# Optimization experiments

Measured on AMD Instinct MI355X. Metric: run time of the kernel, lower is better.

Reference implementation:

```python
import jax, jax.numpy as jnp
import numpy as np

H, D = 4, 8          # heads, per-head dim (hidden=32)
HID = 32
NA = 300_000         # addr nodes
NT = 300_000         # tx nodes
E_IN, E_OUT, E_SP = 1_000_000, 1_000_000, 500_000
NLAYERS = 4
NREL = 3


def setup_inputs() -> dict:
    key = jax.random.key(0)
    ks = iter(jax.random.split(key, 40))
    s = 0.1
    inp = {}
    inp['x_addr'] = jax.random.normal(next(ks), (NA, 53), jnp.float32)
    inp['x_tx'] = jax.random.normal(next(ks), (NT, 6), jnp.float32)
    inp['ei_input'] = jax.random.randint(next(ks), (2, E_IN), 0, NA, jnp.int32)   # addr -> tx
    inp['ei_output'] = jax.random.randint(next(ks), (2, E_OUT), 0, NT, jnp.int32)  # tx -> addr
    inp['ei_spent'] = jax.random.randint(next(ks), (2, E_SP), 0, NT, jnp.int32)   # tx -> tx
    # node encoders
    inp['enc_w_addr'] = jax.random.normal(next(ks), (53, HID), jnp.float32) * s
    inp['enc_b_addr'] = jnp.zeros((HID,), jnp.float32)
    inp['enc_w_tx'] = jax.random.normal(next(ks), (6, HID), jnp.float32) * s
    inp['enc_b_tx'] = jnp.zeros((HID,), jnp.float32)
    # layer norms (shared across layers as in the source)
    inp['ln_addr_g'] = jnp.ones((HID,), jnp.float32)
    inp['ln_addr_b'] = jnp.zeros((HID,), jnp.float32)
    inp['ln_tx_g'] = jnp.ones((HID,), jnp.float32)
    inp['ln_tx_b'] = jnp.zeros((HID,), jnp.float32)
    # 4 HANConv layers, params stacked on leading layer axis
    inp['proj_w_addr'] = jax.random.normal(next(ks), (NLAYERS, HID, HID), jnp.float32) * s
    inp['proj_b_addr'] = jnp.zeros((NLAYERS, HID), jnp.float32)
    inp['proj_w_tx'] = jax.random.normal(next(ks), (NLAYERS, HID, HID), jnp.float32) * s
    inp['proj_b_tx'] = jnp.zeros((NLAYERS, HID), jnp.float32)
    inp['att_src'] = jax.random.normal(next(ks), (NLAYERS, NREL, H, D), jnp.float32) * s
    inp['att_dst'] = jax.random.normal(next(ks), (NLAYERS, NREL, H, D), jnp.float32) * s
    inp['klin_w'] = jax.random.normal(next(ks), (NLAYERS, HID, HID), jnp.float32) * s
    inp['klin_b'] = jnp.zeros((NLAYERS, HID), jnp.float32)
    inp['q'] = jax.random.normal(next(ks), (NLAYERS, HID), jnp.float32) * s
    # output head
    inp['lin_w'] = jax.random.normal(next(ks), (HID, 2), jnp.float32) * s
    inp['lin_b'] = jnp.zeros((2,), jnp.float32)
    return inp


def _layernorm(x, g, b, eps=1e-5):
    m = x.mean(-1, keepdims=True)
    v = ((x - m) ** 2).mean(-1, keepdims=True)
    return (x - m) / jnp.sqrt(v + eps) * g + b


def _segment_softmax(alpha, idx, n):
    # alpha: [E, H]; numerically stable softmax over ragged segments (dst nodes)
    amax = jax.ops.segment_max(alpha, idx, num_segments=n)
    amax = jnp.where(jnp.isfinite(amax), amax, 0.0)
    ex = jnp.exp(alpha - amax[idx])
    den = jax.ops.segment_sum(ex, idx, num_segments=n)
    return ex / (den[idx] + 1e-16)


def _han_conv(xa, xt, ei_in, ei_out, ei_sp,
              pw_a, pb_a, pw_t, pb_t, a_src, a_dst, kw, kb, q):
    h_a = (xa @ pw_a + pb_a).reshape(-1, H, D)   # [NA,H,D]
    h_t = (xt @ pw_t + pb_t).reshape(-1, H, D)   # [NT,H,D]
    rels = [(h_a, h_t, ei_in, 0, 'tx'),     # ('addr','input','tx')
            (h_t, h_a, ei_out, 1, 'addr'),  # ('tx','output','addr')
            (h_t, h_t, ei_sp, 2, 'tx')]     # ('tx','spent_output','tx')
    outs = {'addr': [], 'tx': []}
    for hs, hd, ei, t, dname in rels:
        asrc = (hs * a_src[t]).sum(-1)   # [Ns,H]
        adst = (hd * a_dst[t]).sum(-1)   # [Nd,H]
        si, di = ei[0], ei[1]
        e = jax.nn.leaky_relu(asrc[si] + adst[di], negative_slope=0.2)  # [E,H]
        w = _segment_softmax(e, di, hd.shape[0])                        # [E,H]
        msg = hs[si] * w[:, :, None]                                    # [E,H,D]
        agg = jax.ops.segment_sum(msg, di, num_segments=hd.shape[0])
        outs[dname].append(jax.nn.relu(agg.reshape(-1, H * D)))
    def group(xs):
        out = jnp.stack(xs)                                   # [R,N,F]
        score = (q * jnp.tanh(out @ kw + kb).mean(1)).sum(-1)  # [R]
        attn = jax.nn.softmax(score)
        return (attn[:, None, None] * out).sum(0)
    return group(outs['addr']), group(outs['tx'])


def reference(x_addr, x_tx, ei_input, ei_output, ei_spent,
              enc_w_addr, enc_b_addr, enc_w_tx, enc_b_tx,
              ln_addr_g, ln_addr_b, ln_tx_g, ln_tx_b,
              proj_w_addr, proj_b_addr, proj_w_tx, proj_b_tx,
              att_src, att_dst, klin_w, klin_b, q,
              lin_w, lin_b):
    xa = jax.nn.relu(x_addr @ enc_w_addr + enc_b_addr)
    xt = jax.nn.relu(x_tx @ enc_w_tx + enc_b_tx)
    for l in range(NLAYERS):
        oa, ot = _han_conv(xa, xt, ei_input, ei_output, ei_spent,
                           proj_w_addr[l], proj_b_addr[l],
                           proj_w_tx[l], proj_b_tx[l],
                           att_src[l], att_dst[l],
                           klin_w[l], klin_b[l], q[l])
        xa = _layernorm(jax.nn.relu(oa) + xa, ln_addr_g, ln_addr_b)
        xt = _layernorm(jax.nn.relu(ot) + xt, ln_tx_g, ln_tx_b)
    return xa @ lin_w + lin_b
```

## Files before the change

kernel.cpp:

```cpp
#include <hip/hip_runtime.h>
#include <hip/hip_fp16.h>

#define NLAYERS 4
#define BSHIFT 10
#define CHUNK 4096

typedef _Float16 f16x8 __attribute__((ext_vector_type(8)));
typedef float f32x4 __attribute__((ext_vector_type(4)));

__global__ void zero_int_kernel(int* __restrict__ p, long n) {
    long i = (long)blockIdx.x * 256 + threadIdx.x;
    long stride = (long)gridDim.x * 256;
    for (; i < n; i += stride) p[i] = 0;
}

__device__ __forceinline__ float fast_tanh(float y) {
    y = fminf(fmaxf(y, -15.f), 15.f);
    float t = __expf(2.f * y);
    return (t - 1.f) / (t + 1.f);
}

__device__ __forceinline__ int edge_row(const int* ei_in, const int* ei_out, const int* ei_sp,
                                        int E_IN, int E_OUT, int E_SP, int NT, int NA,
                                        int e, int* src) {
    if (e < E_IN) { *src = ei_in[e]; return ei_in[E_IN + e]; }
    if (e < E_IN + E_OUT) { int i = e - E_IN; *src = ei_out[i]; return NT + ei_out[E_OUT + i]; }
    int i = e - E_IN - E_OUT; *src = ei_sp[i]; return NT + NA + ei_sp[E_SP + i];
}

__global__ void hist_kernel(const int* __restrict__ ei_in, const int* __restrict__ ei_out,
                            const int* __restrict__ ei_sp, int E_IN, int E_OUT, int E_SP,
                            int NT, int NA, int* __restrict__ deg, int E_TOT) {
    int e = blockIdx.x * 256 + threadIdx.x;
    if (e >= E_TOT) return;
    int s;
    int row = edge_row(ei_in, ei_out, ei_sp, E_IN, E_OUT, E_SP, NT, NA, e, &s);
    atomicAdd(&deg[row], 1);
}

__global__ void scatter_kernel(const int* __restrict__ ei_in, const int* __restrict__ ei_out,
                               const int* __restrict__ ei_sp, int E_IN, int E_OUT, int E_SP,
                               int NT, int NA, int* __restrict__ cursor, int* __restrict__ col,
                               int E_TOT) {
    int e = blockIdx.x * 256 + threadIdx.x;
    if (e >= E_TOT) return;
    int s;
    int row = edge_row(ei_in, ei_out, ei_sp, E_IN, E_OUT, E_SP, NT, NA, e, &s);
    int pos = atomicAdd(&cursor[row], 1);
    col[pos] = s;
}

__global__ void scan1_kernel(const int* __restrict__ deg, int* __restrict__ rowptr,
                             int* __restrict__ bsum, int n) {
    __shared__ int lds[256];
    int tid = threadIdx.x;
    int base = blockIdx.x * 1024;
    int v[4];
    int mysum = 0;
    #pragma unroll
    for (int j = 0; j < 4; j++) {
        int idx = base + tid * 4 + j;
        v[j] = (idx < n) ? deg[idx] : 0;
        mysum += v[j];
    }
    lds[tid] = mysum;
    __syncthreads();
    for (int off = 1; off < 256; off <<= 1) {
        int t = (tid >= off) ? lds[tid - off] : 0;
        __syncthreads();
        lds[tid] += t;
        __syncthreads();
    }
    int excl = lds[tid] - mysum;
    if (tid == 255) bsum[blockIdx.x] = lds[tid];
    int run = excl;
    #pragma unroll
    for (int j = 0; j < 4; j++) {
        int idx = base + tid * 4 + j;
        if (idx < n) rowptr[idx] = run;
        run += v[j];
    }
}

__global__ void scan2_kernel(int* __restrict__ bsum, int nb) {
    __shared__ int lds[1024];
    int tid = threadIdx.x;
    int v = (tid < nb) ? bsum[tid] : 0;
    lds[tid] = v;
    __syncthreads();
    for (int off = 1; off < 1024; off <<= 1) {
        int t = (tid >= off) ? lds[tid - off] : 0;
        __syncthreads();
        lds[tid] += t;
        __syncthreads();
    }
    if (tid < nb) bsum[tid] = lds[tid] - v;
}

__global__ void scan3_kernel(int* __restrict__ rowptr, const int* __restrict__ bsum,
                             int* __restrict__ cursor, int n, int E) {
    int i = blockIdx.x * 256 + threadIdx.x;
    if (i < n) {
        int r = rowptr[i] + bsum[i >> 10];
        rowptr[i] = r;
        cursor[i] = r;
    }
    if (i == 0) rowptr[n] = E;
}

__global__ void __launch_bounds__(256) bucket_scatter_kernel(
    const int* __restrict__ ei_in, const int* __restrict__ ei_out,
    const int* __restrict__ ei_sp, int E_IN, int E_OUT, int E_SP,
    int NT, int NA, int* __restrict__ bcur,
    uint2* __restrict__ ebuf, int E_TOT, int nbuck, int cap) {
    __shared__ int lc[1024], lbase[1024], lcur[1024];
    int tid = threadIdx.x;
    int chunk0 = blockIdx.x * CHUNK;
    int chunkN = E_TOT - chunk0;
    if (chunkN > CHUNK) chunkN = CHUNK;
    if (chunkN <= 0) return;
    for (int i = tid; i < nbuck; i += 256) { lc[i] = 0; lcur[i] = 0; }
    __syncthreads();
    uint2 er[CHUNK / 256];
    #pragma unroll
    for (int j = 0; j < CHUNK / 256; j++) {
        int i = tid + j * 256;
        if (i < chunkN) {
            int s;
            int row = edge_row(ei_in, ei_out, ei_sp, E_IN, E_OUT, E_SP, NT, NA, chunk0 + i, &s);
            er[j] = make_uint2((unsigned)row, (unsigned)s);
            atomicAdd(&lc[row >> BSHIFT], 1);
        } else {
            er[j].x = 0xFFFFFFFFu;
        }
    }
    __syncthreads();
    for (int i = tid; i < nbuck; i += 256) if (lc[i]) lbase[i] = atomicAdd(&bcur[i], lc[i]);
    __syncthreads();
    #pragma unroll
    for (int j = 0; j < CHUNK / 256; j++) {
        if (er[j].x != 0xFFFFFFFFu) {
            int b = (int)(er[j].x >> BSHIFT);
            int pos = lbase[b] + atomicAdd(&lcur[b], 1);
            if (pos < cap) ebuf[(size_t)b * cap + pos] = er[j];
        }
    }
}

__global__ void scanb_kernel(const int* __restrict__ bcur, int* __restrict__ boff,
                             int* __restrict__ rowptr, int nbuck, int cap, int NCAT) {
    __shared__ int lds[1024];
    int tid = threadIdx.x;
    int v = 0;
    if (tid < nbuck) { v = bcur[tid]; if (v > cap) v = cap; }
    lds[tid] = v;
    __syncthreads();
    for (int off = 1; off < 1024; off <<= 1) {
        int t = (tid >= off) ? lds[tid - off] : 0;
        __syncthreads();
        lds[tid] += t;
        __syncthreads();
    }
    if (tid < nbuck) boff[tid] = lds[tid] - v;
    if (tid == 1023) {
        boff[nbuck] = lds[1023];
        rowptr[NCAT] = lds[1023];
    }
}

__global__ void __launch_bounds__(256) bucket_csr_kernel(
    const uint2* __restrict__ ebuf, const int* __restrict__ boff,
    int* __restrict__ rowptr, int* __restrict__ col, int NCAT, int cap) {
    __shared__ int ldeg[1024];
    __shared__ int lsum[256];
    int tid = threadIdx.x;
    int b = blockIdx.x;
    int row0 = b << BSHIFT;
    int e0 = boff[b], e1 = boff[b + 1];
    int cnt = e1 - e0;
    const uint2* src = ebuf + (size_t)b * cap;
    for (int i = tid; i < 1024; i += 256) ldeg[i] = 0;
    __syncthreads();
    for (int i = tid; i < cnt; i += 256)
        atomicAdd(&ldeg[src[i].x - (unsigned)row0], 1);
    __syncthreads();
    int bidx = tid * 4;
    int v0 = ldeg[bidx], v1 = ldeg[bidx + 1], v2 = ldeg[bidx + 2], v3 = ldeg[bidx + 3];
    int mysum = v0 + v1 + v2 + v3;
    lsum[tid] = mysum;
    __syncthreads();
    for (int off = 1; off < 256; off <<= 1) {
        int t = (tid >= off) ? lsum[tid - off] : 0;
        __syncthreads();
        lsum[tid] += t;
        __syncthreads();
    }
    int run = e0 + lsum[tid] - mysum;
    int vv[4] = {v0, v1, v2, v3};
    #pragma unroll
    for (int j = 0; j < 4; j++) {
        int r = bidx + j;
        if (row0 + r < NCAT) rowptr[row0 + r] = run;
        ldeg[r] = run;
        run += vv[j];
    }
    __syncthreads();
    for (int i = tid; i < cnt; i += 256) {
        uint2 p = src[i];
        int pos = atomicAdd(&ldeg[p.x - (unsigned)row0], 1);
        col[pos] = (int)p.y;
    }
}

__global__ void __launch_bounds__(256) encproj_addr_kernel(
    const float* __restrict__ x,
    const float* __restrict__ We, const float* __restrict__ be,
    const float* __restrict__ Wp, const float* __restrict__ bp,
    const float* __restrict__ a0, const float* __restrict__ a1,
    float* __restrict__ xa, __half* __restrict__ h,
    __half* __restrict__ o0, float* __restrict__ o1,
    int n, int gpb) {
    __shared__ __align__(16) float lds_t[4][16][36];
    __shared__ float sx[4][16 * 57];
    int tid = threadIdx.x;
    int wave = tid >> 6, lane = tid & 63;
    int colid = lane & 15, kgrp = lane >> 4;
    int fbase = kgrp * 8;

    f16x8 bE00, bE01, bE10, bE11;
    #pragma unroll
    for (int j = 0; j < 8; j++) {
        int k0 = fbase + j;
        int k1 = 32 + fbase + j;
        bE00[j] = (_Float16)We[k0 * 32 + colid];
        bE01[j] = (_Float16)We[k0 * 32 + 16 + colid];
        float w10 = (k1 < 53) ? We[k1 * 32 + colid] : 0.f;
        float w11 = (k1 < 53) ? We[k1 * 32 + 16 + colid] : 0.f;
        bE10[j] = (_Float16)w10;
        bE11[j] = (_Float16)w11;
    }
    float beC0 = be[colid], beC1 = be[16 + colid];

    f16x8 bP0, bP1;
    #pragma unroll
    for (int j = 0; j < 8; j++) {
        bP0[j] = (_Float16)Wp[(fbase + j) * 32 + colid];
        bP1[j] = (_Float16)Wp[(fbase + j) * 32 + 16 + colid];
    }
    float bpC0 = bp[colid], bpC1 = bp[16 + colid];

    float va0[8], va1[8];
    #pragma unroll
    for (int j = 0; j < 8; j++) { va0[j] = a0[fbase + j]; va1[j] = a1[fbase + j]; }

    float (*tp)[36] = lds_t[wave];
    float* sxw = sx[wave];
    int blockBase = blockIdx.x * gpb * 64;
    for (int gi = 0; gi < gpb; gi++) {
        int node0 = blockBase + gi * 64 + wave * 16;
        int node = node0 + colid;
        bool valid = node < n;
        int nn = n - node0;
        if (nn > 16) nn = 16;
        if (nn < 0) nn = 0;
        int elems = nn * 53;
        for (int i = lane; i < elems; i += 64) {
            int r = i / 53, c = i - r * 53;
            sxw[r * 57 + c] = x[(size_t)node0 * 53 + i];
        }
        f16x8 af0, af1;
        #pragma unroll
        for (int j = 0; j < 8; j++) {
            af0[j] = (_Float16)sxw[colid * 57 + fbase + j];
            int kk = 32 + fbase + j;
            float v1 = (kk < 53) ? sxw[colid * 57 + kk] : 0.f;
            af1[j] = (_Float16)v1;
        }
        f32x4 c0 = {0.f, 0.f, 0.f, 0.f};
        f32x4 c1 = {0.f, 0.f, 0.f, 0.f};
        c0 = __builtin_amdgcn_mfma_f32_16x16x32_f16(af0, bE00, c0, 0, 0, 0);
        c0 = __builtin_amdgcn_mfma_f32_16x16x32_f16(af1, bE10, c0, 0, 0, 0);
        c1 = __builtin_amdgcn_mfma_f32_16x16x32_f16(af0, bE01, c1, 0, 0, 0);
        c1 = __builtin_amdgcn_mfma_f32_16x16x32_f16(af1, bE11, c1, 0, 0, 0);
        #pragma unroll
        for (int r = 0; r < 4; r++) {
            c0[r] = fmaxf(c0[r] + beC0, 0.f);
            c1[r] = fmaxf(c1[r] + beC1, 0.f);
        }
        #pragma unroll
        for (int r = 0; r < 4; r++) {
            int row = kgrp * 4 + r;
            tp[row][colid] = c0[r];
            tp[row][16 + colid] = c1[r];
        }
        float4 xlo = *(const float4*)&tp[colid][fbase];
        float4 xhi = *(const float4*)&tp[colid][fbase + 4];
        float xe[8] = {xlo.x, xlo.y, xlo.z, xlo.w, xhi.x, xhi.y, xhi.z, xhi.w};
        if (valid) {
            size_t basep = (size_t)node * 32 + fbase;
            *(float4*)(xa + basep) = xlo;
            *(float4*)(xa + basep + 4) = xhi;
        }
        f16x8 af;
        #pragma unroll
        for (int j = 0; j < 8; j++) af[j] = (_Float16)xe[j];
        f32x4 p0 = {0.f, 0.f, 0.f, 0.f};
        f32x4 p1 = {0.f, 0.f, 0.f, 0.f};
        p0 = __builtin_amdgcn_mfma_f32_16x16x32_f16(af, bP0, p0, 0, 0, 0);
        p1 = __builtin_amdgcn_mfma_f32_16x16x32_f16(af, bP1, p1, 0, 0, 0);
        #pragma unroll
        for (int r = 0; r < 4; r++) { p0[r] += bpC0; p1[r] += bpC1; }
        #pragma unroll
        for (int r = 0; r < 4; r++) {
            int row = kgrp * 4 + r;
            tp[row][colid] = p0[r];
            tp[row][16 + colid] = p1[r];
        }
        float4 hlo = *(const float4*)&tp[colid][fbase];
        float4 hhi = *(const float4*)&tp[colid][fbase + 4];
        float hv[8] = {hlo.x, hlo.y, hlo.z, hlo.w, hhi.x, hhi.y, hhi.z, hhi.w};
        if (valid) {
            float4 hout;
            __half2* hp2 = (__half2*)&hout;
            hp2[0] = __floats2half2_rn(hv[0], hv[1]);
            hp2[1] = __floats2half2_rn(hv[2], hv[3]);
            hp2[2] = __floats2half2_rn(hv[4], hv[5]);
            hp2[3] = __floats2half2_rn(hv[6], hv[7]);
            *(float4*)(h + (size_t)node * 32 + fbase) = hout;
            float d0 = 0.f, d1 = 0.f;
            #pragma unroll
            for (int j = 0; j < 8; j++) {
                d0 += hv[j] * va0[j];
                d1 += hv[j] * va1[j];
            }
            size_t oidx = (size_t)node * 4 + kgrp;
            o0[oidx] = __float2half(d0);
            o1[oidx] = d1;
        }
    }
}

__global__ void __launch_bounds__(256) encproj_tx_kernel(
    const float* __restrict__ x,
    const float* __restrict__ We, const float* __restrict__ be,
    const float* __restrict__ Wp, const float* __restrict__ bp,
    const float* __restrict__ a0, const float* __restrict__ a1,
    const float* __restrict__ a2, const float* __restrict__ a3,
    float* __restrict__ xt, __half* __restrict__ h,
    __half* __restrict__ o0, float* __restrict__ o1,
    __half* __restrict__ o2, float* __restrict__ o3,
    int n, int gpb) {
    __shared__ __align__(16) float lds_t[4][16][36];
    int tid = threadIdx.x;
    int wave = tid >> 6, lane = tid & 63;
    int colid = lane & 15, kgrp = lane >> 4;
    int fbase = kgrp * 8;

    f16x8 bE0, bE1;
    #pragma unroll
    for (int j = 0; j < 8; j++) {
        int k = fbase + j;
        float w0 = (k < 6) ? We[k * 32 + colid] : 0.f;
        float w1 = (k < 6) ? We[k * 32 + 16 + colid] : 0.f;
        bE0[j] = (_Float16)w0;
        bE1[j] = (_Float16)w1;
    }
    float beC0 = be[colid], beC1 = be[16 + colid];

    f16x8 bP0, bP1;
    #pragma unroll
    for (int j = 0; j < 8; j++) {
        bP0[j] = (_Float16)Wp[(fbase + j) * 32 + colid];
        bP1[j] = (_Float16)Wp[(fbase + j) * 32 + 16 + colid];
    }
    float bpC0 = bp[colid], bpC1 = bp[16 + colid];

    float va0[8], va1[8], va2[8], va3[8];
    #pragma unroll
    for (int j = 0; j < 8; j++) {
        va0[j] = a0[fbase + j]; va1[j] = a1[fbase + j];
        va2[j] = a2[fbase + j]; va3[j] = a3[fbase + j];
    }

    float (*tp)[36] = lds_t[wave];
    int blockBase = blockIdx.x * gpb * 64;
    for (int gi = 0; gi < gpb; gi++) {
        int node = blockBase + gi * 64 + wave * 16 + colid;
        bool valid = node < n;
        f16x8 af0;
        #pragma unroll
        for (int j = 0; j < 8; j++) {
            int k = fbase + j;
            float xv = 0.f;
            if (k < 6 && valid) xv = x[(size_t)node * 6 + k];
            af0[j] = (_Float16)xv;
        }
        f32x4 c0 = {0.f, 0.f, 0.f, 0.f};
        f32x4 c1 = {0.f, 0.f, 0.f, 0.f};
        c0 = __builtin_amdgcn_mfma_f32_16x16x32_f16(af0, bE0, c0, 0, 0, 0);
        c1 = __builtin_amdgcn_mfma_f32_16x16x32_f16(af0, bE1, c1, 0, 0, 0);
        #pragma unroll
        for (int r = 0; r < 4; r++) {
            c0[r] = fmaxf(c0[r] + beC0, 0.f);
            c1[r] = fmaxf(c1[r] + beC1, 0.f);
        }
        #pragma unroll
        for (int r = 0; r < 4; r++) {
            int row = kgrp * 4 + r;
            tp[row][colid] = c0[r];
            tp[row][16 + colid] = c1[r];
        }
        float4 xlo = *(const float4*)&tp[colid][fbase];
        float4 xhi = *(const float4*)&tp[colid][fbase + 4];
        float xe[8] = {xlo.x, xlo.y, xlo.z, xlo.w, xhi.x, xhi.y, xhi.z, xhi.w};
        if (valid) {
            size_t basep = (size_t)node * 32 + fbase;
            *(float4*)(xt + basep) = xlo;
            *(float4*)(xt + basep + 4) = xhi;
        }
        f16x8 af;
        #pragma unroll
        for (int j = 0; j < 8; j++) af[j] = (_Float16)xe[j];
        f32x4 p0 = {0.f, 0.f, 0.f, 0.f};
        f32x4 p1 = {0.f, 0.f, 0.f, 0.f};
        p0 = __builtin_amdgcn_mfma_f32_16x16x32_f16(af, bP0, p0, 0, 0, 0);
        p1 = __builtin_amdgcn_mfma_f32_16x16x32_f16(af, bP1, p1, 0, 0, 0);
        #pragma unroll
        for (int r = 0; r < 4; r++) { p0[r] += bpC0; p1[r] += bpC1; }
        #pragma unroll
        for (int r = 0; r < 4; r++) {
            int row = kgrp * 4 + r;
            tp[row][colid] = p0[r];
            tp[row][16 + colid] = p1[r];
        }
        float4 hlo = *(const float4*)&tp[colid][fbase];
        float4 hhi = *(const float4*)&tp[colid][fbase + 4];
        float hv[8] = {hlo.x, hlo.y, hlo.z, hlo.w, hhi.x, hhi.y, hhi.z, hhi.w};
        if (valid) {
            float4 hout;
            __half2* hp2 = (__half2*)&hout;
            hp2[0] = __floats2half2_rn(hv[0], hv[1]);
            hp2[1] = __floats2half2_rn(hv[2], hv[3]);
            hp2[2] = __floats2half2_rn(hv[4], hv[5]);
            hp2[3] = __floats2half2_rn(hv[6], hv[7]);
            *(float4*)(h + (size_t)node * 32 + fbase) = hout;
            float d0 = 0.f, d1 = 0.f, d2 = 0.f, d3 = 0.f;
            #pragma unroll
            for (int j = 0; j < 8; j++) {
                d0 += hv[j] * va0[j];
                d1 += hv[j] * va1[j];
                d2 += hv[j] * va2[j];
                d3 += hv[j] * va3[j];
            }
            size_t oidx = (size_t)node * 4 + kgrp;
            o0[oidx] = __float2half(d0);
            o1[oidx] = d1;
            o2[oidx] = __float2half(d2);
            o3[oidx] = d3;
        }
    }
}

__global__ void agg_all_kernel(
    const int* __restrict__ rowptr, const int* __restrict__ col,
    const __half* __restrict__ h_a, const __half* __restrict__ h_t,
    const __half* __restrict__ asrc0, const float* __restrict__ adst0,
    const __half* __restrict__ asrc1, const float* __restrict__ adst1,
    const __half* __restrict__ asrc2, const float* __restrict__ adst2,
    __half* __restrict__ agg_t0, __half* __restrict__ agg_a, __half* __restrict__ agg_t2,
    const float* __restrict__ kw, const float* __restrict__ kb, const float* __restrict__ q,
    float* __restrict__ scoreOut, int NT, int NA, int mode, int nRows) {
    __shared__ float sW[1024];
    __shared__ float sb[32];
    __shared__ float sq[32];
    __shared__ float sScore[2];
    int tid = threadIdx.x;
    bool doScore = (mode != 2);
    if (doScore) {
        for (int i = tid; i < 1024; i += 256) sW[i] = kw[i];
        if (tid < 32) { sb[tid] = kb[tid]; sq[tid] = q[tid]; }
        if (tid < 2) sScore[tid] = 0.f;
        __syncthreads();
    }
    int lane = tid & 3;
    int f0 = lane * 8;
    long stride = (long)gridDim.x * 64;
    for (long gi = (long)blockIdx.x * 64 + (tid >> 2); gi < (long)nRows; gi += stride) {
        int row;
        if (mode == 0) row = (int)gi;
        else if (mode == 1) row = (gi < NT) ? (int)gi : (int)(gi + NA);
        else row = NT + (int)gi;
        int rel, dst;
        const __half* h; const __half* asrc; const float* adp; __half* agg;
        if (row < NT)           { rel = 0; dst = row;           h = h_a; asrc = asrc0; adp = adst0; agg = agg_t0; }
        else if (row < NT + NA) { rel = 1; dst = row - NT;      h = h_t; asrc = asrc1; adp = adst1; agg = agg_a; }
        else                    { rel = 2; dst = row - NT - NA; h = h_t; asrc = asrc2; adp = adst2; agg = agg_t2; }
        float ad = adp[dst * 4 + lane];
        int e0 = rowptr[row], e1 = rowptr[row + 1];
        __half2 acc0 = __floats2half2_rn(0.f, 0.f);
        __half2 acc1 = acc0, acc2 = acc0, acc3 = acc0;
        float den = 0.f;
        for (int e = e0; e < e1; e += 4) {
            int s0 = col[e];
            int s1 = (e + 1 < e1) ? col[e + 1] : s0;
            int s2 = (e + 2 < e1) ? col[e + 2] : s0;
            int s3 = (e + 3 < e1) ? col[e + 3] : s0;
            float as0 = __half2float(asrc[s0 * 4 + lane]);
            float as1 = __half2float(asrc[s1 * 4 + lane]);
            float as2 = __half2float(asrc[s2 * 4 + lane]);
            float as3 = __half2float(asrc[s3 * 4 + lane]);
            float4 r0 = *(const float4*)(h + s0 * 32 + f0);
            float4 r1 = *(const float4*)(h + s1 * 32 + f0);
            float4 r2 = *(const float4*)(h + s2 * 32 + f0);
            float4 r3 = *(const float4*)(h + s3 * 32 + f0);
            float t0 = as0 + ad; t0 = t0 > 0.f ? t0 : 0.2f * t0;
            float t1 = as1 + ad; t1 = t1 > 0.f ? t1 : 0.2f * t1;
            float t2 = as2 + ad; t2 = t2 > 0.f ? t2 : 0.2f * t2;
            float t3 = as3 + ad; t3 = t3 > 0.f ? t3 : 0.2f * t3;
            float ex0 = __expf(t0);
            float ex1 = (e + 1 < e1) ? __expf(t1) : 0.f;
            float ex2 = (e + 2 < e1) ? __expf(t2) : 0.f;
            float ex3 = (e + 3 < e1) ? __expf(t3) : 0.f;
            den += (ex0 + ex1) + (ex2 + ex3);
            __half2 eh0 = __float2half2_rn(ex0), eh1 = __float2half2_rn(ex1);
            __half2 eh2 = __float2half2_rn(ex2), eh3 = __float2half2_rn(ex3);
            const __half2* h0 = (const __half2*)&r0;
            const __half2* h1 = (const __half2*)&r1;
            const __half2* h2 = (const __half2*)&r2;
            const __half2* h3 = (const __half2*)&r3;
            acc0 = __hfma2(eh0, h0[0], acc0);
            acc1 = __hfma2(eh0, h0[1], acc1);
            acc2 = __hfma2(eh0, h0[2], acc2);
            acc3 = __hfma2(eh0, h0[3], acc3);
            acc0 = __hfma2(eh1, h1[0], acc0);
            acc1 = __hfma2(eh1, h1[1], acc1);
            acc2 = __hfma2(eh1, h1[2], acc2);
            acc3 = __hfma2(eh1, h1[3], acc3);
            acc0 = __hfma2(eh2, h2[0], acc0);
            acc1 = __hfma2(eh2, h2[1], acc1);
            acc2 = __hfma2(eh2, h2[2], acc2);
            acc3 = __hfma2(eh2, h2[3], acc3);
            acc0 = __hfma2(eh3, h3[0], acc0);
            acc1 = __hfma2(eh3, h3[1], acc1);
            acc2 = __hfma2(eh3, h3[2], acc2);
            acc3 = __hfma2(eh3, h3[3], acc3);
        }
        float r = 1.f / (den + 1e-16f);
        float2 a0 = __half22float2(acc0), a1 = __half22float2(acc1);
        float2 a2 = __half22float2(acc2), a3 = __half22float2(acc3);
        float v[8] = {a0.x * r, a0.y * r, a1.x * r, a1.y * r,
                      a2.x * r, a2.y * r, a3.x * r, a3.y * r};
        float4 opack;
        __half2* op2 = (__half2*)&opack;
        op2[0] = __floats2half2_rn(v[0], v[1]);
        op2[1] = __floats2half2_rn(v[2], v[3]);
        op2[2] = __floats2half2_rn(v[4], v[5]);
        op2[3] = __floats2half2_rn(v[6], v[7]);
        *(float4*)(agg + dst * 32 + f0) = opack;
        if (doScore && rel != 1) {
            float rv[8];
            #pragma unroll
            for (int j = 0; j < 8; j++) rv[j] = fmaxf(v[j], 0.f);
            float y[8];
            #pragma unroll
            for (int j = 0; j < 8; j++) y[j] = sb[f0 + j];
            #pragma unroll
            for (int g = 0; g < 4; g++) {
                float c[8];
                #pragma unroll
                for (int jj = 0; jj < 8; jj++) c[jj] = __shfl(rv[jj], g, 4);
                int kb8 = g * 8;
                #pragma unroll
                for (int jj = 0; jj < 8; jj++) {
                    #pragma unroll
                    for (int j = 0; j < 8; j++)
                        y[j] += c[jj] * sW[(kb8 + jj) * 32 + f0 + j];
                }
            }
            float sacc = 0.f;
            #pragma unroll
            for (int j = 0; j < 8; j++) sacc += sq[f0 + j] * fast_tanh(y[j]);
            sacc += __shfl_xor(sacc, 1, 4);
            sacc += __shfl_xor(sacc, 2, 4);
            if (lane == 0) atomicAdd(&sScore[rel == 2 ? 1 : 0], sacc);
        }
    }
    if (doScore) {
        __syncthreads();
        if (tid < 2) unsafeAtomicAdd(scoreOut + tid, sScore[tid]);
    }
}

__global__ void __launch_bounds__(256) combineproj_kernel(
    const __half* __restrict__ agg_a, const __half* __restrict__ agg_t0, const __half* __restrict__ agg_t2,
    float* __restrict__ xa, float* __restrict__ xt,
    const float* __restrict__ ln_ag, const float* __restrict__ ln_ab,
    const float* __restrict__ ln_tg, const float* __restrict__ ln_tb,
    const float* __restrict__ scores, float invNT,
    const float* __restrict__ Wa, const float* __restrict__ Ba,
    const float* __restrict__ Wt, const float* __restrict__ Bt,
    const float* __restrict__ as0, const float* __restrict__ ad1,
    const float* __restrict__ as1, const float* __restrict__ ad0,
    const float* __restrict__ as2, const float* __restrict__ ad2,
    __half* __restrict__ h_a, __half* __restrict__ h_t,
    __half* __restrict__ o_as0, float* __restrict__ o_ad1,
    __half* __restrict__ o_as1, float* __restrict__ o_ad0,
    __half* __restrict__ o_as2, float* __restrict__ o_ad2,
    int NA_, int NT_, int nbAcp, int gpb, int lastProj) {
    __shared__ __align__(16) float lds_t[4][16][36];
    int tid = threadIdx.x;
    int wave = tid >> 6;
    int lane = tid & 63;
    int colid = lane & 15;
    int kgrp = lane >> 4;
    int fbase = kgrp * 8;

    bool isA = blockIdx.x < (unsigned)nbAcp;
    const float* W = isA ? Wa : Wt;
    const float* Bp = isA ? Ba : Bt;
    int n = isA ? NA_ : NT_;

    f16x8 bf0, bf1;
    #pragma unroll
    for (int j = 0; j < 8; j++) {
        bf0[j] = (_Float16)W[(fbase + j) * 32 + colid];
        bf1[j] = (_Float16)W[(fbase + j) * 32 + 16 + colid];
    }
    float bp0 = Bp[colid], bp1 = Bp[16 + colid];

    const float* lng = isA ? ln_ag : ln_tg;
    const float* lnb = isA ? ln_ab : ln_tb;
    float g[8], bb[8];
    #pragma unroll
    for (int j = 0; j < 8; j++) { g[j] = lng[fbase + j]; bb[j] = lnb[fbase + j]; }

    float va0[8], va1[8], va2[8], va3[8];
    if (isA) {
        #pragma unroll
        for (int j = 0; j < 8; j++) { va0[j] = as0[fbase + j]; va1[j] = ad1[fbase + j]; }
    } else {
        #pragma unroll
        for (int j = 0; j < 8; j++) {
            va0[j] = as1[fbase + j]; va1[j] = ad0[fbase + j];
            va2[j] = as2[fbase + j]; va3[j] = ad2[fbase + j];
        }
    }

    float wsem0 = 0.f, wsem2 = 0.f;
    if (!isA) {
        float s0 = scores[0] * invNT, s2 = scores[1] * invNT;
        float mx = fmaxf(s0, s2);
        float e0 = __expf(s0 - mx), e2 = __expf(s2 - mx);
        float inv_s = 1.f / (e0 + e2);
        wsem0 = e0 * inv_s; wsem2 = e2 * inv_s;
    }

    float (*tp)[36] = lds_t[wave];
    int blockBase = (isA ? (int)blockIdx.x : (int)blockIdx.x - nbAcp) * gpb * 64;
    for (int gi = 0; gi < gpb; gi++) {
        int node = blockBase + gi * 64 + wave * 16 + colid;
        bool valid = node < n;
        float v[8];
        if (valid) {
            size_t base = (size_t)node * 32 + fbase;
            float4 xlo, xhi;
            if (isA) {
                xlo = *(const float4*)(xa + base);
                xhi = *(const float4*)(xa + base + 4);
                float4 ar = *(const float4*)(agg_a + base);
                const __half2* ah2 = (const __half2*)&ar;
                float2 f0 = __half22float2(ah2[0]);
                float2 f1 = __half22float2(ah2[1]);
                float2 f2 = __half22float2(ah2[2]);
                float2 f3 = __half22float2(ah2[3]);
                float av[8] = {f0.x, f0.y, f1.x, f1.y, f2.x, f2.y, f3.x, f3.y};
                float xv[8] = {xlo.x, xlo.y, xlo.z, xlo.w, xhi.x, xhi.y, xhi.z, xhi.w};
                #pragma unroll
                for (int j = 0; j < 8; j++) v[j] = fmaxf(av[j], 0.f) + xv[j];
            } else {
                xlo = *(const float4*)(xt + base);
                xhi = *(const float4*)(xt + base + 4);
                float4 a0r = *(const float4*)(agg_t0 + base);
                float4 a2r = *(const float4*)(agg_t2 + base);
                const __half2* a0h = (const __half2*)&a0r;
                const __half2* a2h = (const __half2*)&a2r;
                float xv[8] = {xlo.x, xlo.y, xlo.z, xlo.w, xhi.x, xhi.y, xhi.z, xhi.w};
                #pragma unroll
                for (int j = 0; j < 4; j++) {
                    float2 p0 = __half22float2(a0h[j]);
                    float2 p2 = __half22float2(a2h[j]);
                    float c0 = wsem0 * fmaxf(p0.x, 0.f) + wsem2 * fmaxf(p2.x, 0.f);
                    float c1 = wsem0 * fmaxf(p0.y, 0.f) + wsem2 * fmaxf(p2.y, 0.f);
                    v[2 * j]     = fmaxf(c0, 0.f) + xv[2 * j];
                    v[2 * j + 1] = fmaxf(c1, 0.f) + xv[2 * j + 1];
                }
            }
        } else {
            #pragma unroll
            for (int j = 0; j < 8; j++) v[j] = 0.f;
        }
        float s = 0.f;
        #pragma unroll
        for (int j = 0; j < 8; j++) s += v[j];
        s += __shfl_xor(s, 16, 64);
        s += __shfl_xor(s, 32, 64);
        float m = s * 0.03125f;
        float d[8], vv = 0.f;
        #pragma unroll
        for (int j = 0; j < 8; j++) { d[j] = v[j] - m; vv += d[j] * d[j]; }
        vv += __shfl_xor(vv, 16, 64);
        vv += __shfl_xor(vv, 32, 64);
        float inv = 1.f / sqrtf(vv * 0.03125f + 1e-5f);
        float ln[8];
        #pragma unroll
        for (int j = 0; j < 8; j++) ln[j] = d[j] * inv * g[j] + bb[j];

        if (valid && (isA || !lastProj)) {
            float* xp = isA ? xa : xt;
            size_t base = (size_t)node * 32 + fbase;
            *(float4*)(xp + base)     = make_float4(ln[0], ln[1], ln[2], ln[3]);
            *(float4*)(xp + base + 4) = make_float4(ln[4], ln[5], ln[6], ln[7]);
        }

        f16x8 af;
        #pragma unroll
        for (int j = 0; j < 8; j++) af[j] = (_Float16)ln[j];
        f32x4 c0 = {0.f, 0.f, 0.f, 0.f};
        f32x4 c1 = {0.f, 0.f, 0.f, 0.f};
        c0 = __builtin_amdgcn_mfma_f32_16x16x32_f16(af, bf0, c0, 0, 0, 0);
        c1 = __builtin_amdgcn_mfma_f32_16x16x32_f16(af, bf1, c1, 0, 0, 0);
        #pragma unroll
        for (int r = 0; r < 4; r++) { c0[r] += bp0; c1[r] += bp1; }

        #pragma unroll
        for (int r = 0; r < 4; r++) {
            int row = kgrp * 4 + r;
            tp[row][colid] = c0[r];
            tp[row][16 + colid] = c1[r];
        }
        float4 hlo = *(const float4*)&tp[colid][fbase];
        float4 hhi = *(const float4*)&tp[colid][fbase + 4];
        float hv[8] = {hlo.x, hlo.y, hlo.z, hlo.w, hhi.x, hhi.y, hhi.z, hhi.w};

        bool writeH = (!isA || !lastProj);
        if (valid && writeH) {
            float4 hout;
            __half2* hp2 = (__half2*)&hout;
            hp2[0] = __floats2half2_rn(hv[0], hv[1]);
            hp2[1] = __floats2half2_rn(hv[2], hv[3]);
            hp2[2] = __floats2half2_rn(hv[4], hv[5]);
            hp2[3] = __floats2half2_rn(hv[6], hv[7]);
            __half* hp = isA ? h_a : h_t;
            *(float4*)(hp + (size_t)node * 32 + fbase) = hout;
        }

        if (valid) {
            size_t oidx = (size_t)node * 4 + kgrp;
            if (isA) {
                if (!lastProj) {
                    float ds = 0.f;
                    #pragma unroll
                    for (int j = 0; j < 8; j++) ds += hv[j] * va0[j];
                    o_as0[oidx] = __float2half(ds);
                }
                float dd = 0.f;
                #pragma unroll
                for (int j = 0; j < 8; j++) dd += hv[j] * va1[j];
                o_ad1[oidx] = dd;
            } else {
                float d0 = 0.f;
                #pragma unroll
                for (int j = 0; j < 8; j++) d0 += hv[j] * va0[j];
                o_as1[oidx] = __float2half(d0);
                if (!lastProj) {
                    float d1 = 0.f, d2 = 0.f, d3 = 0.f;
                    #pragma unroll
                    for (int j = 0; j < 8; j++) {
                        d1 += hv[j] * va1[j];
                        d2 += hv[j] * va2[j];
                        d3 += hv[j] * va3[j];
                    }
                    o_ad0[oidx] = d1;
                    o_as2[oidx] = __float2half(d2);
                    o_ad2[oidx] = d3;
                }
            }
        }
    }
}

__global__ void combine_final_kernel(const __half* __restrict__ agg_a, const float* __restrict__ xa,
                                     const float* __restrict__ g, const float* __restrict__ bt,
                                     const float* __restrict__ lw, const float* __restrict__ lb,
                                     float* __restrict__ out, int n) {
    int tid = threadIdx.x;
    int local = tid >> 5, f = tid & 31;
    int node = blockIdx.x * 8 + local;
    if (node >= n) return;
    float a = __half2float(agg_a[(size_t)node * 32 + f]);
    float v = fmaxf(a, 0.f) + xa[(size_t)node * 32 + f];
    float m = v;
    #pragma unroll
    for (int mask = 1; mask < 32; mask <<= 1) m += __shfl_xor(m, mask, 64);
    m *= (1.f / 32.f);
    float d = v - m;
    float var = d * d;
    #pragma unroll
    for (int mask = 1; mask < 32; mask <<= 1) var += __shfl_xor(var, mask, 64);
    var *= (1.f / 32.f);
    float inv = 1.f / sqrtf(var + 1e-5f);
    float ln = d * inv * g[f] + bt[f];
    float p0 = ln * lw[f * 2 + 0];
    float p1 = ln * lw[f * 2 + 1];
    #pragma unroll
    for (int mask = 1; mask < 32; mask <<= 1) {
        p0 += __shfl_xor(p0, mask, 64);
        p1 += __shfl_xor(p1, mask, 64);
    }
    if (f == 0) {
        out[(size_t)node * 2 + 0] = p0 + lb[0];
        out[(size_t)node * 2 + 1] = p1 + lb[1];
    }
}

extern "C" void kernel_launch(void* const* d_in, const int* in_sizes, int n_in,
                              void* d_out, int out_size, void* d_ws, size_t ws_size,
                              hipStream_t stream) {
    const float* x_addr = (const float*)d_in[0];
    const float* x_tx   = (const float*)d_in[1];
    const int* ei_in    = (const int*)d_in[2];
    const int* ei_out   = (const int*)d_in[3];
    const int* ei_sp    = (const int*)d_in[4];
    const float* enc_w_addr = (const float*)d_in[5];
    const float* enc_b_addr = (const float*)d_in[6];
    const float* enc_w_tx   = (const float*)d_in[7];
    const float* enc_b_tx   = (const float*)d_in[8];
    const float* ln_ag = (const float*)d_in[9];
    const float* ln_ab = (const float*)d_in[10];
    const float* ln_tg = (const float*)d_in[11];
    const float* ln_tb = (const float*)d_in[12];
    const float* pw_a = (const float*)d_in[13];
    const float* pb_a = (const float*)d_in[14];
    const float* pw_t = (const float*)d_in[15];
    const float* pb_t = (const float*)d_in[16];
    const float* att_src = (const float*)d_in[17];
    const float* att_dst = (const float*)d_in[18];
    const float* klw = (const float*)d_in[19];
    const float* klb = (const float*)d_in[20];
    const float* qv  = (const float*)d_in[21];
    const float* lin_w = (const float*)d_in[22];
    const float* lin_b = (const float*)d_in[23];
    float* out = (float*)d_out;

    const int NA = in_sizes[0] / 53;
    const int NT = in_sizes[1] / 6;
    const int E_IN = in_sizes[2] / 2;
    const int E_OUT = in_sizes[3] / 2;
    const int E_SP = in_sizes[4] / 2;
    const int E_TOT = E_IN + E_OUT + E_SP;
    const int NCAT = NT + NA + NT;
    const int NBUCK = (NCAT + (1 << BSHIFT) - 1) >> BSHIFT;

    size_t off = 0;
    float* base = (float*)d_ws;
    auto alloc = [&](size_t nfloats) {
        float* p = base + off;
        off += (nfloats + 63) & ~(size_t)63;
        return p;
    };
    float* xa      = alloc((size_t)NA * 32);
    float* xt      = alloc((size_t)NT * 32);
    float* agg_a_f = alloc((size_t)NA * 16);
    float* agg_t0f = alloc((size_t)NT * 16);
    float* agg_t2f = alloc((size_t)NT * 16);
    float* h_t_f   = alloc((size_t)NT * 16);
    float* asrc0a  = alloc((size_t)NA * 2);
    float* adst1a  = alloc((size_t)NA * 4);
    float* asrc1t  = alloc((size_t)NT * 2);
    float* adst0t  = alloc((size_t)NT * 4);
    float* asrc2t  = alloc((size_t)NT * 2);
    float* adst2t  = alloc((size_t)NT * 4);
    int* rowptrAll = (int*)alloc((size_t)NCAT + 64);
    int* colAll    = (int*)alloc((size_t)E_TOT);
    size_t tmp_span = (((size_t)NCAT + 63) & ~(size_t)63) + 1088 + 64 + 1024;
    int* tmp       = (int*)alloc((size_t)NCAT);
    int* bsum      = (int*)alloc(1088);
    float* scores  = alloc(64);
    int* bcur      = (int*)alloc(1024);
    int* boff      = (int*)alloc(1088);

    size_t ha_floats = (((size_t)NA * 16) + 63) & ~(size_t)63;
    bool roomy = ((off + ha_floats) * sizeof(float)) <= ws_size;
    float* h_a_f = roomy ? alloc((size_t)NA * 16) : agg_a_f;

    int avgb = (int)(((long)E_TOT << BSHIFT) / (long)NCAT);
    int cap = ((avgb + avgb / 4 + 256) + 255) & ~255;
    size_t ebuf_floats = (size_t)NBUCK * (size_t)cap * 2;
    bool canBucket = (NBUCK <= 1024) &&
                     (((off + ebuf_floats + 64) * sizeof(float)) <= ws_size);
    uint2* ebuf = canBucket ? (uint2*)alloc(ebuf_floats) : nullptr;

    __half* agg_a  = (__half*)agg_a_f;
    __half* agg_t0 = (__half*)agg_t0f;
    __half* agg_t2 = (__half*)agg_t2f;
    __half* h_t    = (__half*)h_t_f;
    __half* h_a    = (__half*)h_a_f;
    __half* has0   = (__half*)asrc0a;
    __half* has1   = (__half*)asrc1t;
    __half* has2   = (__half*)asrc2t;

    dim3 blk(256);
    const int GPB_E = 4;
    const int GPB_C = 4;
    int nbA8 = (NA + 7) / 8;
    int nbAe = (NA + 64 * GPB_E - 1) / (64 * GPB_E);
    int nbTe = (NT + 64 * GPB_E - 1) / (64 * GPB_E);
    int nbAcp = (NA + 64 * GPB_C - 1) / (64 * GPB_C);
    int nbTcp = (NT + 64 * GPB_C - 1) / (64 * GPB_C);
    int nbE = (E_TOT + 255) / 256;
    int nbScan = (NCAT + 1023) / 1024;

    if (canBucket) {
        int nbChunk = (E_TOT + CHUNK - 1) / CHUNK;
        zero_int_kernel<<<8, blk, 0, stream>>>((int*)scores, 64 + 1024);
        bucket_scatter_kernel<<<nbChunk, blk, 0, stream>>>(
            ei_in, ei_out, ei_sp, E_IN, E_OUT, E_SP, NT, NA, bcur, ebuf, E_TOT, NBUCK, cap);
        scanb_kernel<<<1, 1024, 0, stream>>>(bcur, boff, rowptrAll, NBUCK, cap, NCAT);
        bucket_csr_kernel<<<NBUCK, blk, 0, stream>>>(ebuf, boff, rowptrAll, colAll, NCAT, cap);
    } else {
        zero_int_kernel<<<2048, blk, 0, stream>>>(tmp, (long)tmp_span);
        hist_kernel<<<nbE, blk, 0, stream>>>(ei_in, ei_out, ei_sp, E_IN, E_OUT, E_SP, NT, NA, tmp, E_TOT);
        scan1_kernel<<<nbScan, blk, 0, stream>>>(tmp, rowptrAll, bsum, NCAT);
        scan2_kernel<<<1, 1024, 0, stream>>>(bsum, nbScan);
        scan3_kernel<<<(NCAT + 255) / 256, blk, 0, stream>>>(rowptrAll, bsum, tmp, NCAT, E_TOT);
        scatter_kernel<<<nbE, blk, 0, stream>>>(ei_in, ei_out, ei_sp, E_IN, E_OUT, E_SP, NT, NA, tmp, colAll, E_TOT);
    }

    encproj_addr_kernel<<<nbAe, blk, 0, stream>>>(
        x_addr, enc_w_addr, enc_b_addr, pw_a, pb_a,
        att_src + 0 * 32, att_dst + 1 * 32,
        xa, h_a, has0, adst1a, NA, GPB_E);
    encproj_tx_kernel<<<nbTe, blk, 0, stream>>>(
        x_tx, enc_w_tx, enc_b_tx, pw_t, pb_t,
        att_src + 1 * 32, att_dst + 0 * 32, att_src + 2 * 32, att_dst + 2 * 32,
        xt, h_t, has1, adst0t, has2, adst2t, NT, GPB_E);

    auto agg_launch = [&](int mode, int nRows, const float* kw, const float* kb,
                          const float* q, float* sc) {
        int blocks = (nRows + 63) / 64;
        if (blocks > 2048) blocks = 2048;
        agg_all_kernel<<<blocks, blk, 0, stream>>>(
            rowptrAll, colAll, h_a, h_t,
            has0, adst0t, has1, adst1a, has2, adst2t,
            agg_t0, agg_a, agg_t2, kw, kb, q, sc, NT, NA, mode, nRows);
    };

    for (int l = 0; l < NLAYERS; l++) {
        bool last = (l == NLAYERS - 1);
        const float* kw = klw + l * 1024;
        const float* kb = klb + l * 32;
        const float* q  = qv + l * 32;
        float* sc = scores + 2 * l;
        if (!last) {
            if (roomy) {
                agg_launch(0, NCAT, kw, kb, q, sc);
            } else {
                agg_launch(1, 2 * NT, kw, kb, q, sc);
                agg_launch(2, NA, kw, kb, q, sc);
            }
            int lp = l + 1;
            combineproj_kernel<<<nbAcp + nbTcp, blk, 0, stream>>>(
                agg_a, agg_t0, agg_t2, xa, xt,
                ln_ag, ln_ab, ln_tg, ln_tb,
                sc, 1.0f / (float)NT,
                pw_a + lp * 1024, pb_a + lp * 32, pw_t + lp * 1024, pb_t + lp * 32,
                att_src + (lp * 3 + 0) * 32, att_dst + (lp * 3 + 1) * 32,
                att_src + (lp * 3 + 1) * 32, att_dst + (lp * 3 + 0) * 32,
                att_src + (lp * 3 + 2) * 32, att_dst + (lp * 3 + 2) * 32,
                h_a, h_t,
                has0, adst1a, has1, adst0t, has2, adst2t,
                NA, NT, nbAcp, GPB_C, lp == 3 ? 1 : 0);
        } else {
            agg_launch(2, NA, kw, kb, q, sc);
            combine_final_kernel<<<nbA8, blk, 0, stream>>>(agg_a, xa, ln_ag, ln_ab,
                                                           lin_w, lin_b, out, NA);
        }
    }
}
```

Before: 729.6 us.

## Compute semantic-attention score projection with MFMA inside aggregation kernel

Replaces the scalar per-row 32x32 projection (LDS weights plus shuffles) used for the relation-level attention score with two 16x16x32 fp16 MFMA ops per 16-row wave tile. Fragments are gathered via a lane shuffle, and score partials are accumulated in registers and reduced across the wave once at the end, instead of one LDS atomic per row. This removes the heavy FMA and LDS traffic of the score path. In exchange the loop is restructured around 16-row wave tiles with padded invalid rows, and the projection runs in fp16.

```diff
diff --git a/kernel.cpp b/kernel.cpp
--- a/kernel.cpp
+++ b/kernel.cpp
@@ -461,7 +461,7 @@
     }
 }
 
-__global__ void agg_all_kernel(
+__global__ void __launch_bounds__(256) agg_all_kernel(
     const int* __restrict__ rowptr, const int* __restrict__ col,
     const __half* __restrict__ h_a, const __half* __restrict__ h_t,
     const __half* __restrict__ asrc0, const float* __restrict__ adst0,
@@ -470,31 +470,44 @@
     __half* __restrict__ agg_t0, __half* __restrict__ agg_a, __half* __restrict__ agg_t2,
     const float* __restrict__ kw, const float* __restrict__ kb, const float* __restrict__ q,
     float* __restrict__ scoreOut, int NT, int NA, int mode, int nRows) {
-    __shared__ float sW[1024];
-    __shared__ float sb[32];
-    __shared__ float sq[32];
     __shared__ float sScore[2];
     int tid = threadIdx.x;
     bool doScore = (mode != 2);
+    if (tid < 2) sScore[tid] = 0.f;
+    __syncthreads();
+    int lane64 = tid & 63;
+    int wave = tid >> 6;
+    int lane = tid & 3;
+    int wr = lane64 >> 2;
+    int f0 = lane * 8;
+    int colid = lane64 & 15, kgrp = lane64 >> 4;
+    f16x8 bK0 = {}, bK1 = {};
+    float kb0 = 0.f, kb1 = 0.f, q0 = 0.f, q1 = 0.f;
     if (doScore) {
-        for (int i = tid; i < 1024; i += 256) sW[i] = kw[i];
-        if (tid < 32) { sb[tid] = kb[tid]; sq[tid] = q[tid]; }
-        if (tid < 2) sScore[tid] = 0.f;
-        __syncthreads();
-    }
-    int lane = tid & 3;
-    int f0 = lane * 8;
+        #pragma unroll
+        for (int j = 0; j < 8; j++) {
+            bK0[j] = (_Float16)kw[(kgrp * 8 + j) * 32 + colid];
+            bK1[j] = (_Float16)kw[(kgrp * 8 + j) * 32 + 16 + colid];
+        }
+        kb0 = kb[colid]; kb1 = kb[16 + colid];
+        q0 = q[colid];  q1 = q[16 + colid];
+    }
+    int srcl = ((lane64 & 15) << 2) | (lane64 >> 4);
+    float s0acc = 0.f, s2acc = 0.f;
     long stride = (long)gridDim.x * 64;
-    for (long gi = (long)blockIdx.x * 64 + (tid >> 2); gi < (long)nRows; gi += stride) {
+    for (long wbase = (long)blockIdx.x * 64 + wave * 16; wbase < (long)nRows; wbase += stride) {
+        long gi = wbase + wr;
+        bool valid = gi < (long)nRows;
+        long gc = valid ? gi : (long)nRows - 1;
         int row;
-        if (mode == 0) row = (int)gi;
-        else if (mode == 1) row = (gi < NT) ? (int)gi : (int)(gi + NA);
-        else row = NT + (int)gi;
-        int rel, dst;
+        if (mode == 0) row = (int)gc;
+        else if (mode == 1) row = (gc < NT) ? (int)gc : (int)(gc + NA);
+        else row = NT + (int)gc;
+        int dst;
         const __half* h; const __half* asrc; const float* adp; __half* agg;
-        if (row < NT)           { rel = 0; dst = row;           h = h_a; asrc = asrc0; adp = adst0; agg = agg_t0; }
-        else if (row < NT + NA) { rel = 1; dst = row - NT;      h = h_t; asrc = asrc1; adp = adst1; agg = agg_a; }
-        else                    { rel = 2; dst = row - NT - NA; h = h_t; asrc = asrc2; adp = adst2; agg = agg_t2; }
+        if (row < NT)           { dst = row;           h = h_a; asrc = asrc0; adp = adst0; agg = agg_t0; }
+        else if (row < NT + NA) { dst = row - NT;      h = h_t; asrc = asrc1; adp = adst1; agg = agg_a; }
+        else                    { dst = row - NT - NA; h = h_t; asrc = asrc2; adp = adst2; agg = agg_t2; }
         float ad = adp[dst * 4 + lane];
         int e0 = rowptr[row], e1 = rowptr[row + 1];
         __half2 acc0 = __floats2half2_rn(0.f, 0.f);
@@ -556,36 +569,56 @@
         op2[1] = __floats2half2_rn(v[2], v[3]);
         op2[2] = __floats2half2_rn(v[4], v[5]);
         op2[3] = __floats2half2_rn(v[6], v[7]);
-        *(float4*)(agg + dst * 32 + f0) = opack;
-        if (doScore && rel != 1) {
-            float rv[8];
-            #pragma unroll
-            for (int j = 0; j < 8; j++) rv[j] = fmaxf(v[j], 0.f);
-            float y[8];
-            #pragma unroll
-            for (int j = 0; j < 8; j++) y[j] = sb[f0 + j];
-            #pragma unroll
-            for (int g = 0; g < 4; g++) {
-                float c[8];
+        if (valid) *(float4*)(agg + dst * 32 + f0) = opack;
+        if (doScore) {
+            bool skipAll = (mode == 0) && (wbase >= (long)NT) && (wbase + 15 < (long)NT + NA);
+            if (!skipAll) {
+                float z = 0.f;
+                __half2 ph0 = __floats2half2_rn(valid ? fmaxf(v[0], z) : z, valid ? fmaxf(v[1], z) : z);
+                __half2 ph1 = __floats2half2_rn(valid ? fmaxf(v[2], z) : z, valid ? fmaxf(v[3], z) : z);
+                __half2 ph2 = __floats2half2_rn(valid ? fmaxf(v[4], z) : z, valid ? fmaxf(v[5], z) : z);
+                __half2 ph3 = __floats2half2_rn(valid ? fmaxf(v[6], z) : z, valid ? fmaxf(v[7], z) : z);
+                int4 uu;
+                uu.x = __shfl(*(int*)&ph0, srcl, 64);
+                uu.y = __shfl(*(int*)&ph1, srcl, 64);
+                uu.z = __shfl(*(int*)&ph2, srcl, 64);
+                uu.w = __shfl(*(int*)&ph3, srcl, 64);
+                f16x8 afrag = *(f16x8*)&uu;
+                f32x4 y0 = {0.f, 0.f, 0.f, 0.f};
+                f32x4 y1 = {0.f, 0.f, 0.f, 0.f};
+                y0 = __builtin_amdgcn_mfma_f32_16x16x32_f16(afrag, bK0, y0, 0, 0, 0);
+                y1 = __builtin_amdgcn_mfma_f32_16x16x32_f16(afrag, bK1, y1, 0, 0, 0);
                 #pragma unroll
-                for (int jj = 0; jj < 8; jj++) c[jj] = __shfl(rv[jj], g, 4);
-                int kb8 = g * 8;
-                #pragma unroll
-                for (int jj = 0; jj < 8; jj++) {
-                    #pragma unroll
-                    for (int j = 0; j < 8; j++)
-                        y[j] += c[jj] * sW[(kb8 + jj) * 32 + f0 + j];
+                for (int rr = 0; rr < 4; rr++) {
+                    long gr = wbase + (long)(kgrp * 4 + rr);
+                    if (gr < (long)nRows) {
+                        bool isRel1, b0;
+                        if (mode == 0) {
+                            isRel1 = (gr >= (long)NT) && (gr < (long)NT + NA);
+                            b0 = gr < (long)NT;
+                        } else {
+                            isRel1 = false;
+                            b0 = gr < (long)NT;
+                        }
+                        if (!isRel1) {
+                            float t = q0 * fast_tanh(y0[rr] + kb0) + q1 * fast_tanh(y1[rr] + kb1);
+                            if (b0) s0acc += t; else s2acc += t;
+                        }
+                    }
                 }
             }
-            float sacc = 0.f;
-            #pragma unroll
-            for (int j = 0; j < 8; j++) sacc += sq[f0 + j] * fast_tanh(y[j]);
-            sacc += __shfl_xor(sacc, 1, 4);
-            sacc += __shfl_xor(sacc, 2, 4);
-            if (lane == 0) atomicAdd(&sScore[rel == 2 ? 1 : 0], sacc);
         }
     }
     if (doScore) {
+        #pragma unroll
+        for (int m = 1; m < 64; m <<= 1) {
+            s0acc += __shfl_xor(s0acc, m, 64);
+            s2acc += __shfl_xor(s2acc, m, 64);
+        }
+        if (lane64 == 0) {
+            atomicAdd(&sScore[0], s0acc);
+            atomicAdd(&sScore[1], s2acc);
+        }
         __syncthreads();
         if (tid < 2) unsafeAtomicAdd(scoreOut + tid, sScore[tid]);
     }
```

Result: no change. 722.2 us (-1.0%).
